# Kernel optimization log

Hardware: AMD Instinct MI355X
Metric: run time of the kernel (lower is better)

The kernel has to match this reference:

```python
import jax, jax.numpy as jnp
import numpy as np

BIG = 1e30  # stand-in for +inf at DP boundaries (never selected by min)


def setup_inputs() -> dict:
    key = jax.random.key(0)
    kx, kp = jax.random.split(key)
    B, D, T = 32, 16, 1024        # batch, channels (d_patts), stream length
    P, L = 64, 32                 # n_patts, l_patts
    x = jax.random.normal(kx, (B, D, T), dtype=jnp.float32)
    patts = jax.random.normal(kp, (P, D, L), dtype=jnp.float32)
    rho = 0.5
    w = float(rho ** (1.0 / L))   # self.w = rho ** (1 / l_patts)
    return {"x": x, "patts": patts, "w": w}


def _dtw(x, patts, w):
    # Weighted streaming DTW: for each pattern p and each ending time j,
    # D[i, j] = cost[i, j] + min(D[i-1, j], w*D[i, j-1], w*D[i-1, j-1])
    # with D[i, 0] = cost[i, 0] + D[i-1, 0] (first time column cumsum) and
    # cost[i, j] = ||x[:, j] - patts[:, i]||^2 (squared euclidean over channels).
    B, D, T = x.shape
    P, _, L = patts.shape
    p2 = jnp.sum(patts * patts, axis=1)                       # (P, L)

    def cost_at(xj):                                          # xj: (B, D)
        x2 = jnp.sum(xj * xj, axis=1)                         # (B,)
        xp = jnp.einsum('bd,pdl->bpl', xj, patts)             # (B, P, L)
        return x2[:, None, None] + p2[None] - 2.0 * xp        # (B, P, L)

    # first time column
    col0 = jnp.cumsum(cost_at(x[:, :, 0]), axis=-1)           # (B, P, L)

    def step(prev, xj):
        cost = cost_at(xj)                                    # (B, P, L)
        prev_up = jnp.concatenate(
            [jnp.full_like(prev[..., :1], BIG), prev[..., :-1]], axis=-1)
        m = w * jnp.minimum(prev, prev_up)                    # (B, P, L)

        def inner(new_im1, cm):                               # scan along pattern axis
            c_i, m_i = cm
            new_i = c_i + jnp.minimum(new_im1, m_i)
            return new_i, new_i

        _, new = jax.lax.scan(
            inner, jnp.full((B, P), BIG, cost.dtype),
            (jnp.moveaxis(cost, -1, 0), jnp.moveaxis(m, -1, 0)))
        new_col = jnp.moveaxis(new, 0, -1)                    # (B, P, L)
        return new_col, new_col[..., -1]                      # emit full-pattern match cost

    xs = jnp.moveaxis(x[:, :, 1:], -1, 0)                     # (T-1, B, D)
    _, rest = jax.lax.scan(step, col0, xs)                    # (T-1, B, P)
    dtw = jnp.concatenate([col0[None, ..., -1], rest], axis=0)  # (T, B, P)
    return jnp.moveaxis(dtw, 0, -1)                           # (B, P, T)


def reference(x, patts, w):
    return jnp.sqrt(_dtw(x, patts, w))
```

## Files before the change

kernel.cpp:

```cpp
#include <hip/hip_runtime.h>
#include <math.h>

#define B_ 32
#define D_ 16
#define T_ 1024
#define P_ 64
#define L_ 32
#define KB 524288.0f

typedef short short8 __attribute__((ext_vector_type(8)));
typedef float f32x4 __attribute__((ext_vector_type(4)));
typedef unsigned short ushort_t;

template<int CTRL, int ROW_MASK, bool BC>
__device__ __forceinline__ float dpp_mov(float old_, float src) {
  int o = __builtin_bit_cast(int, old_);
  int s = __builtin_bit_cast(int, src);
  int r = __builtin_amdgcn_update_dpp(o, s, CTRL, ROW_MASK, 0xf, BC);
  return __builtin_bit_cast(float, r);
}

__device__ __forceinline__ float scan_sum32(float v) {
  v += dpp_mov<0x111, 0xf, true>(0.f, v);
  v += dpp_mov<0x112, 0xf, true>(0.f, v);
  v += dpp_mov<0x114, 0xf, true>(0.f, v);
  v += dpp_mov<0x118, 0xf, true>(0.f, v);
  v += dpp_mov<0x142, 0xa, false>(0.f, v);
  return v;
}

__device__ __forceinline__ float scan_max32(float v) {
  asm("s_nop 1\n\t"
      "v_max_f32_dpp %0, %0, %0 row_shr:1 row_mask:0xf bank_mask:0xf\n\t"
      "s_nop 1\n\t"
      "v_max_f32_dpp %0, %0, %0 row_shr:2 row_mask:0xf bank_mask:0xf\n\t"
      "s_nop 1\n\t"
      "v_max_f32_dpp %0, %0, %0 row_shr:4 row_mask:0xf bank_mask:0xf\n\t"
      "s_nop 1\n\t"
      "v_max_f32_dpp %0, %0, %0 row_shr:8 row_mask:0xf bank_mask:0xf\n\t"
      "s_nop 1\n\t"
      "v_max_f32_dpp %0, %0, %0 row_bcast:15 row_mask:0xa bank_mask:0xf"
      : "+v"(v));
  return v;
}

__device__ __forceinline__ ushort_t f2bf(float f) {
  unsigned u = __builtin_bit_cast(unsigned, f);
  return (ushort_t)((u + 0x7FFFu + ((u >> 16) & 1u)) >> 16);
}
__device__ __forceinline__ float bf2f(ushort_t h) {
  unsigned u = ((unsigned)h) << 16;
  return __builtin_bit_cast(float, u);
}

__global__ __launch_bounds__(256) void prep_fused(
    const float* __restrict__ x, const float* __restrict__ patts,
    ushort_t* __restrict__ xA, ushort_t* __restrict__ pB) {
  const int bid = blockIdx.x;
  if (bid < 128) {
    int gid = bid * 256 + threadIdx.x;
    int b = gid >> 10, t = gid & 1023;
    float x2 = 0.f;
    ushort_t o[32];
#pragma unroll
    for (int d = 0; d < 16; ++d) {
      float v = x[((b * 16 + d) << 10) + t];
      x2 = fmaf(v, v, x2);
      o[d] = f2bf(v);
    }
    o[16] = 0x3F80; o[17] = 0x3F80;
    ushort_t hi = f2bf(x2);
    o[18] = hi;
    o[19] = f2bf(x2 - bf2f(hi));
#pragma unroll
    for (int d = 20; d < 32; ++d) o[d] = 0;
    uint4* dst = (uint4*)(xA + (size_t)gid * 32);
#pragma unroll
    for (int q = 0; q < 4; ++q) {
      const ushort_t* s = o + q * 8;
      uint4 u;
      u.x = (unsigned)s[0] | ((unsigned)s[1] << 16);
      u.y = (unsigned)s[2] | ((unsigned)s[3] << 16);
      u.z = (unsigned)s[4] | ((unsigned)s[5] << 16);
      u.w = (unsigned)s[6] | ((unsigned)s[7] << 16);
      dst[q] = u;
    }
  } else {
    __shared__ float Ls[4][16 * 33];
    __shared__ float Lh[4][64];
    __shared__ float LP2[4][32];
    const int sub = threadIdx.x >> 6;
    const int l = threadIdx.x & 63;
    const int p = (bid - 128) * 4 + sub;
    const int half = l >> 5;
    const int m = l & 31;

    float p2acc = 0.f;
#pragma unroll
    for (int dd = 0; dd < 16; dd += 2) {
      int d = dd + half;
      float v = patts[((p * 16 + d) << 5) + m];
      p2acc = fmaf(v, v, p2acc);
      Ls[sub][d * 33 + m] = scan_sum32(v);
    }
    Lh[sub][l] = p2acc;
    __syncthreads();
    {
      float tot = Lh[sub][m] + Lh[sub][32 + m];
      float pref = scan_sum32(tot);
      if (half == 0) LP2[sub][m] = pref;
    }
    __syncthreads();

    const int n = l & 15, q = l >> 4;
#pragma unroll
    for (int iblk = 0; iblk < 2; ++iblk) {
      const int i = iblk * 16 + n;
      ushort_t o[8];
      if (q < 2) {
#pragma unroll
        for (int e = 0; e < 8; ++e)
          o[e] = f2bf(-2.f * Ls[sub][(q * 8 + e) * 33 + i]);
      } else if (q == 2) {
        float P2 = LP2[sub][i];
        ushort_t hi = f2bf(P2);
        o[0] = hi; o[1] = f2bf(P2 - bf2f(hi));
        o[2] = f2bf((float)(i + 1)); o[3] = o[2];
        o[4] = o[5] = o[6] = o[7] = 0;
      } else {
#pragma unroll
        for (int e = 0; e < 8; ++e) o[e] = 0;
      }
      uint4 u;
      u.x = (unsigned)o[0] | ((unsigned)o[1] << 16);
      u.y = (unsigned)o[2] | ((unsigned)o[3] << 16);
      u.z = (unsigned)o[4] | ((unsigned)o[5] << 16);
      u.w = (unsigned)o[6] | ((unsigned)o[7] << 16);
      ((uint4*)pB)[(p * 2 + iblk) * 64 + l] = u;
    }
  }
}

__global__ __launch_bounds__(256, 4) void dtw_kernel(
    const ushort_t* __restrict__ xA,
    const ushort_t* __restrict__ pBg,
    const float* __restrict__ wp,
    float* __restrict__ out)
{
  __shared__ float lds[4 * 1320];

  const int tid = threadIdx.x;
  const int l   = tid & 63;
  const int wid = tid >> 6;
  const int li  = l & 31;
  const int g   = l >> 5;
  const int q4  = l >> 4;
  const unsigned bx = blockIdx.x;
  const int ch   = bx & 3u;
  const unsigned rest = bx >> 2;
  const int b     = rest >> 3;
  const int pbase = (rest & 7) << 3;
  const int pA  = pbase + (wid << 1);
  const float w = wp[0];
  const float nw = -w;
  const bool l0c = (li == 0), l31 = (li == 31);

  const int S0    = ch * 12;
  const int nT    = 28;
  const int warmT = ch ? 16 : 0;

  const short8* pBs = (const short8*)pBg;
  short8 B00 = pBs[((pA    ) * 2 + 0) * 64 + l];
  short8 B01 = pBs[((pA    ) * 2 + 1) * 64 + l];
  short8 B10 = pBs[((pA + 1) * 2 + 0) * 64 + l];
  short8 B11 = pBs[((pA + 1) * 2 + 1) * 64 + l];

  const short8* xAs = (const short8*)xA + ((size_t)b << 12);

  short8 Aa;
  auto loadA = [&](int t) {
    Aa = xAs[((((S0 + t) << 4) + (l & 15)) << 2) + q4];
  };

  float* base = lds + wid * 1320;
  float* ldsW = base + 20 + (l & 15) * 20 + q4 * 4;
  const float* ldsR  = base + 20 + g * 660 + li * 20;
  const float* ldsRx = ldsR - 20;

  if (l < 20) { base[l] = KB; base[660 + l] = KB; }
  __syncthreads();

  const f32x4 zk = {KB, KB, KB, KB};

  auto fill = [&]() {
    f32x4 d0 = __builtin_amdgcn_mfma_f32_16x16x32_bf16(Aa, B00, zk, 0, 0, 0);
    f32x4 d1 = __builtin_amdgcn_mfma_f32_16x16x32_bf16(Aa, B01, zk, 0, 0, 0);
    f32x4 d2 = __builtin_amdgcn_mfma_f32_16x16x32_bf16(Aa, B10, zk, 0, 0, 0);
    f32x4 d3 = __builtin_amdgcn_mfma_f32_16x16x32_bf16(Aa, B11, zk, 0, 0, 0);
    *(f32x4*)(ldsW + 0)   = d0;
    *(f32x4*)(ldsW + 320) = d1;
    *(f32x4*)(ldsW + 660) = d2;
    *(f32x4*)(ldsW + 980) = d3;
  };

  float* orow = out + (((size_t)(b * P_ + pA + g)) << 10) + (S0 << 4);
  float dcur = 0.f;

  loadA(0);
  fill();
  loadA(1);

  for (int t = 0; t < nT; ++t) {
    f32x4 s0 = *(const f32x4*)(ldsR + 0);
    f32x4 x0 = *(const f32x4*)(ldsRx + 0);
    f32x4 s1 = *(const f32x4*)(ldsR + 4);
    f32x4 x1 = *(const f32x4*)(ldsRx + 4);
    f32x4 s2 = *(const f32x4*)(ldsR + 8);
    f32x4 x2 = *(const f32x4*)(ldsRx + 8);
    f32x4 s3 = *(const f32x4*)(ldsR + 12);
    f32x4 x3 = *(const f32x4*)(ldsRx + 12);

    if (t + 1 < nT) fill();
    if (t + 2 < nT) loadA(t + 2);

    const bool first = (t == 0);
    const bool store = (t >= warmT);
    float* op = orow + (t << 4);

    float4 r0, r1, r2, r3;
#pragma unroll
    for (int k4 = 0; k4 < 4; ++k4) {
      f32x4 Sq = (k4 == 0) ? s0 : (k4 == 1) ? s1 : (k4 == 2) ? s2 : s3;
      f32x4 Xq = (k4 == 0) ? x0 : (k4 == 1) ? x1 : (k4 == 2) ? x2 : x3;
      float4 rv;
#pragma unroll
      for (int e = 0; e < 4; ++e) {
        float Zo = Sq[e];
        float Zx = Xq[e];
        float a = fmaf(nw, dcur, Zx);
        float c = fmaf(nw, dcur, Zo);
        float u;
        asm("s_nop 1\n\t"
            "v_max_f32_dpp %0, %1, %2 wave_shr:1 row_mask:0xf bank_mask:0xf"
            : "=&v"(u) : "v"(c), "v"(a));
        u = l0c ? a : u;
        float Mx = scan_max32(u);
        float val = Zo - Mx;
        if (first && k4 == 0 && e == 0)
          val = Zo - KB;
        dcur = val;
        if (e == 0) rv.x = val; else if (e == 1) rv.y = val;
        else if (e == 2) rv.z = val; else rv.w = val;
      }
      if (k4 == 0) r0 = rv; else if (k4 == 1) r1 = rv;
      else if (k4 == 2) r2 = rv; else r3 = rv;
    }
    if (store) {
      if (l31) {
        float4 s;
        s.x = __builtin_amdgcn_sqrtf(r0.x); s.y = __builtin_amdgcn_sqrtf(r0.y);
        s.z = __builtin_amdgcn_sqrtf(r0.z); s.w = __builtin_amdgcn_sqrtf(r0.w);
        *(float4*)(op + 0) = s;
        s.x = __builtin_amdgcn_sqrtf(r1.x); s.y = __builtin_amdgcn_sqrtf(r1.y);
        s.z = __builtin_amdgcn_sqrtf(r1.z); s.w = __builtin_amdgcn_sqrtf(r1.w);
        *(float4*)(op + 4) = s;
        s.x = __builtin_amdgcn_sqrtf(r2.x); s.y = __builtin_amdgcn_sqrtf(r2.y);
        s.z = __builtin_amdgcn_sqrtf(r2.z); s.w = __builtin_amdgcn_sqrtf(r2.w);
        *(float4*)(op + 8) = s;
        s.x = __builtin_amdgcn_sqrtf(r3.x); s.y = __builtin_amdgcn_sqrtf(r3.y);
        s.z = __builtin_amdgcn_sqrtf(r3.z); s.w = __builtin_amdgcn_sqrtf(r3.w);
        *(float4*)(op + 12) = s;
      }
    }
  }
}

extern "C" void kernel_launch(void* const* d_in, const int* in_sizes, int n_in,
                              void* d_out, int out_size, void* d_ws, size_t ws_size,
                              hipStream_t stream) {
  const float* x     = (const float*)d_in[0];
  const float* patts = (const float*)d_in[1];
  const float* w     = (const float*)d_in[2];
  float* out = (float*)d_out;

  ushort_t* xA = (ushort_t*)d_ws;
  ushort_t* pB = (ushort_t*)((char*)d_ws + (size_t)B_ * T_ * 32 * 2);

  prep_fused<<<144, 256, 0, stream>>>(x, patts, xA, pB);
  dtw_kernel<<<B_ * (P_ / 8) * 4, 256, 0, stream>>>(xA, pB, w, out);
}
```

Before: 109.8 us.

## Interleave two independent DTW chains per wave to hide DPP latency

Each wave now processes four patterns as two independent recurrence chains, interleaving their DPP max-scans so one chain's instructions fill the other's data-dependency hazard slots. The s_nop padding drops to zero between paired DPP ops. The grid halves, LDS per block doubles, and the launch-bounds occupancy hint drops from 4 to 2. The cost is fewer waves across the GPU (1024 blocks become 512) and higher register pressure.

```diff
diff --git a/kernel.cpp b/kernel.cpp
--- a/kernel.cpp
+++ b/kernel.cpp
@@ -29,19 +29,23 @@
   return v;
 }
 
-__device__ __forceinline__ float scan_max32(float v) {
+__device__ __forceinline__ void scan_max32_x2(float& u, float& v) {
   asm("s_nop 1\n\t"
       "v_max_f32_dpp %0, %0, %0 row_shr:1 row_mask:0xf bank_mask:0xf\n\t"
-      "s_nop 1\n\t"
+      "v_max_f32_dpp %1, %1, %1 row_shr:1 row_mask:0xf bank_mask:0xf\n\t"
+      "s_nop 0\n\t"
       "v_max_f32_dpp %0, %0, %0 row_shr:2 row_mask:0xf bank_mask:0xf\n\t"
-      "s_nop 1\n\t"
+      "v_max_f32_dpp %1, %1, %1 row_shr:2 row_mask:0xf bank_mask:0xf\n\t"
+      "s_nop 0\n\t"
       "v_max_f32_dpp %0, %0, %0 row_shr:4 row_mask:0xf bank_mask:0xf\n\t"
-      "s_nop 1\n\t"
+      "v_max_f32_dpp %1, %1, %1 row_shr:4 row_mask:0xf bank_mask:0xf\n\t"
+      "s_nop 0\n\t"
       "v_max_f32_dpp %0, %0, %0 row_shr:8 row_mask:0xf bank_mask:0xf\n\t"
-      "s_nop 1\n\t"
-      "v_max_f32_dpp %0, %0, %0 row_bcast:15 row_mask:0xa bank_mask:0xf"
-      : "+v"(v));
-  return v;
+      "v_max_f32_dpp %1, %1, %1 row_shr:8 row_mask:0xf bank_mask:0xf\n\t"
+      "s_nop 0\n\t"
+      "v_max_f32_dpp %0, %0, %0 row_bcast:15 row_mask:0xa bank_mask:0xf\n\t"
+      "v_max_f32_dpp %1, %1, %1 row_bcast:15 row_mask:0xa bank_mask:0xf"
+      : "+v"(u), "+v"(v));
 }
 
 __device__ __forceinline__ ushort_t f2bf(float f) {
@@ -141,13 +145,13 @@
   }
 }
 
-__global__ __launch_bounds__(256, 4) void dtw_kernel(
+__global__ __launch_bounds__(256, 2) void dtw_kernel(
     const ushort_t* __restrict__ xA,
     const ushort_t* __restrict__ pBg,
     const float* __restrict__ wp,
     float* __restrict__ out)
 {
-  __shared__ float lds[4 * 1320];
+  __shared__ float lds[4 * 2640];
 
   const int tid = threadIdx.x;
   const int l   = tid & 63;
@@ -158,9 +162,9 @@
   const unsigned bx = blockIdx.x;
   const int ch   = bx & 3u;
   const unsigned rest = bx >> 2;
-  const int b     = rest >> 3;
-  const int pbase = (rest & 7) << 3;
-  const int pA  = pbase + (wid << 1);
+  const int b     = rest >> 2;
+  const int pbase = (rest & 3) << 4;
+  const int pA0   = pbase + (wid << 2);
   const float w = wp[0];
   const float nw = -w;
   const bool l0c = (li == 0), l31 = (li == 31);
@@ -170,10 +174,14 @@
   const int warmT = ch ? 16 : 0;
 
   const short8* pBs = (const short8*)pBg;
-  short8 B00 = pBs[((pA    ) * 2 + 0) * 64 + l];
-  short8 B01 = pBs[((pA    ) * 2 + 1) * 64 + l];
-  short8 B10 = pBs[((pA + 1) * 2 + 0) * 64 + l];
-  short8 B11 = pBs[((pA + 1) * 2 + 1) * 64 + l];
+  short8 B00 = pBs[((pA0    ) * 2 + 0) * 64 + l];
+  short8 B01 = pBs[((pA0    ) * 2 + 1) * 64 + l];
+  short8 B10 = pBs[((pA0 + 1) * 2 + 0) * 64 + l];
+  short8 B11 = pBs[((pA0 + 1) * 2 + 1) * 64 + l];
+  short8 B20 = pBs[((pA0 + 2) * 2 + 0) * 64 + l];
+  short8 B21 = pBs[((pA0 + 2) * 2 + 1) * 64 + l];
+  short8 B30 = pBs[((pA0 + 3) * 2 + 0) * 64 + l];
+  short8 B31 = pBs[((pA0 + 3) * 2 + 1) * 64 + l];
 
   const short8* xAs = (const short8*)xA + ((size_t)b << 12);
 
@@ -182,12 +190,16 @@
     Aa = xAs[((((S0 + t) << 4) + (l & 15)) << 2) + q4];
   };
 
-  float* base = lds + wid * 1320;
+  float* base = lds + wid * 2640;
   float* ldsW = base + 20 + (l & 15) * 20 + q4 * 4;
-  const float* ldsR  = base + 20 + g * 660 + li * 20;
-  const float* ldsRx = ldsR - 20;
-
-  if (l < 20) { base[l] = KB; base[660 + l] = KB; }
+  const float* ldsRA  = base + 20 + g * 660 + li * 20;
+  const float* ldsRxA = ldsRA - 20;
+  const float* ldsRB  = ldsRA + 1320;
+  const float* ldsRxB = ldsRB - 20;
+
+  if (l < 20) {
+    base[l] = KB; base[660 + l] = KB; base[1320 + l] = KB; base[1980 + l] = KB;
+  }
   __syncthreads();
 
   const f32x4 zk = {KB, KB, KB, KB};
@@ -197,79 +209,123 @@
     f32x4 d1 = __builtin_amdgcn_mfma_f32_16x16x32_bf16(Aa, B01, zk, 0, 0, 0);
     f32x4 d2 = __builtin_amdgcn_mfma_f32_16x16x32_bf16(Aa, B10, zk, 0, 0, 0);
     f32x4 d3 = __builtin_amdgcn_mfma_f32_16x16x32_bf16(Aa, B11, zk, 0, 0, 0);
-    *(f32x4*)(ldsW + 0)   = d0;
-    *(f32x4*)(ldsW + 320) = d1;
-    *(f32x4*)(ldsW + 660) = d2;
-    *(f32x4*)(ldsW + 980) = d3;
+    f32x4 d4 = __builtin_amdgcn_mfma_f32_16x16x32_bf16(Aa, B20, zk, 0, 0, 0);
+    f32x4 d5 = __builtin_amdgcn_mfma_f32_16x16x32_bf16(Aa, B21, zk, 0, 0, 0);
+    f32x4 d6 = __builtin_amdgcn_mfma_f32_16x16x32_bf16(Aa, B30, zk, 0, 0, 0);
+    f32x4 d7 = __builtin_amdgcn_mfma_f32_16x16x32_bf16(Aa, B31, zk, 0, 0, 0);
+    *(f32x4*)(ldsW + 0)    = d0;
+    *(f32x4*)(ldsW + 320)  = d1;
+    *(f32x4*)(ldsW + 660)  = d2;
+    *(f32x4*)(ldsW + 980)  = d3;
+    *(f32x4*)(ldsW + 1320) = d4;
+    *(f32x4*)(ldsW + 1640) = d5;
+    *(f32x4*)(ldsW + 1980) = d6;
+    *(f32x4*)(ldsW + 2300) = d7;
   };
 
-  float* orow = out + (((size_t)(b * P_ + pA + g)) << 10) + (S0 << 4);
-  float dcur = 0.f;
+  float* orowA = out + (((size_t)(b * P_ + pA0 + g)) << 10) + (S0 << 4);
+  float* orowB = orowA + (2 << 10);
+  float dcurA = 0.f, dcurB = 0.f;
 
   loadA(0);
   fill();
   loadA(1);
 
   for (int t = 0; t < nT; ++t) {
-    f32x4 s0 = *(const f32x4*)(ldsR + 0);
-    f32x4 x0 = *(const f32x4*)(ldsRx + 0);
-    f32x4 s1 = *(const f32x4*)(ldsR + 4);
-    f32x4 x1 = *(const f32x4*)(ldsRx + 4);
-    f32x4 s2 = *(const f32x4*)(ldsR + 8);
-    f32x4 x2 = *(const f32x4*)(ldsRx + 8);
-    f32x4 s3 = *(const f32x4*)(ldsR + 12);
-    f32x4 x3 = *(const f32x4*)(ldsRx + 12);
+    f32x4 sA0 = *(const f32x4*)(ldsRA  + 0);
+    f32x4 xA0 = *(const f32x4*)(ldsRxA + 0);
+    f32x4 sB0 = *(const f32x4*)(ldsRB  + 0);
+    f32x4 xB0 = *(const f32x4*)(ldsRxB + 0);
+    f32x4 sA1 = *(const f32x4*)(ldsRA  + 4);
+    f32x4 xA1 = *(const f32x4*)(ldsRxA + 4);
+    f32x4 sB1 = *(const f32x4*)(ldsRB  + 4);
+    f32x4 xB1 = *(const f32x4*)(ldsRxB + 4);
+    f32x4 sA2 = *(const f32x4*)(ldsRA  + 8);
+    f32x4 xA2 = *(const f32x4*)(ldsRxA + 8);
+    f32x4 sB2 = *(const f32x4*)(ldsRB  + 8);
+    f32x4 xB2 = *(const f32x4*)(ldsRxB + 8);
+    f32x4 sA3 = *(const f32x4*)(ldsRA  + 12);
+    f32x4 xA3 = *(const f32x4*)(ldsRxA + 12);
+    f32x4 sB3 = *(const f32x4*)(ldsRB  + 12);
+    f32x4 xB3 = *(const f32x4*)(ldsRxB + 12);
 
     if (t + 1 < nT) fill();
     if (t + 2 < nT) loadA(t + 2);
 
     const bool first = (t == 0);
     const bool store = (t >= warmT);
-    float* op = orow + (t << 4);
-
-    float4 r0, r1, r2, r3;
+
+    float4 rA0, rA1, rA2, rA3, rB0, rB1, rB2, rB3;
 #pragma unroll
     for (int k4 = 0; k4 < 4; ++k4) {
-      f32x4 Sq = (k4 == 0) ? s0 : (k4 == 1) ? s1 : (k4 == 2) ? s2 : s3;
-      f32x4 Xq = (k4 == 0) ? x0 : (k4 == 1) ? x1 : (k4 == 2) ? x2 : x3;
-      float4 rv;
+      f32x4 SqA = (k4 == 0) ? sA0 : (k4 == 1) ? sA1 : (k4 == 2) ? sA2 : sA3;
+      f32x4 XqA = (k4 == 0) ? xA0 : (k4 == 1) ? xA1 : (k4 == 2) ? xA2 : xA3;
+      f32x4 SqB = (k4 == 0) ? sB0 : (k4 == 1) ? sB1 : (k4 == 2) ? sB2 : sB3;
+      f32x4 XqB = (k4 == 0) ? xB0 : (k4 == 1) ? xB1 : (k4 == 2) ? xB2 : xB3;
+      float4 rvA, rvB;
 #pragma unroll
       for (int e = 0; e < 4; ++e) {
-        float Zo = Sq[e];
-        float Zx = Xq[e];
-        float a = fmaf(nw, dcur, Zx);
-        float c = fmaf(nw, dcur, Zo);
-        float u;
+        float ZoA = SqA[e], ZxA = XqA[e];
+        float ZoB = SqB[e], ZxB = XqB[e];
+        float aA = fmaf(nw, dcurA, ZxA);
+        float cA = fmaf(nw, dcurA, ZoA);
+        float aB = fmaf(nw, dcurB, ZxB);
+        float cB = fmaf(nw, dcurB, ZoB);
+        float uA, uB;
         asm("s_nop 1\n\t"
-            "v_max_f32_dpp %0, %1, %2 wave_shr:1 row_mask:0xf bank_mask:0xf"
-            : "=&v"(u) : "v"(c), "v"(a));
-        u = l0c ? a : u;
-        float Mx = scan_max32(u);
-        float val = Zo - Mx;
-        if (first && k4 == 0 && e == 0)
-          val = Zo - KB;
-        dcur = val;
-        if (e == 0) rv.x = val; else if (e == 1) rv.y = val;
-        else if (e == 2) rv.z = val; else rv.w = val;
+            "v_max_f32_dpp %0, %2, %3 wave_shr:1 row_mask:0xf bank_mask:0xf\n\t"
+            "v_max_f32_dpp %1, %4, %5 wave_shr:1 row_mask:0xf bank_mask:0xf"
+            : "=&v"(uA), "=&v"(uB)
+            : "v"(cA), "v"(aA), "v"(cB), "v"(aB));
+        uA = l0c ? aA : uA;
+        uB = l0c ? aB : uB;
+        scan_max32_x2(uA, uB);
+        float vA = ZoA - uA;
+        float vB = ZoB - uB;
+        if (first && k4 == 0 && e == 0) {
+          vA = ZoA - KB;
+          vB = ZoB - KB;
+        }
+        dcurA = vA; dcurB = vB;
+        if (e == 0) { rvA.x = vA; rvB.x = vB; }
+        else if (e == 1) { rvA.y = vA; rvB.y = vB; }
+        else if (e == 2) { rvA.z = vA; rvB.z = vB; }
+        else { rvA.w = vA; rvB.w = vB; }
       }
-      if (k4 == 0) r0 = rv; else if (k4 == 1) r1 = rv;
-      else if (k4 == 2) r2 = rv; else r3 = rv;
+      if (k4 == 0) { rA0 = rvA; rB0 = rvB; }
+      else if (k4 == 1) { rA1 = rvA; rB1 = rvB; }
+      else if (k4 == 2) { rA2 = rvA; rB2 = rvB; }
+      else { rA3 = rvA; rB3 = rvB; }
     }
     if (store) {
       if (l31) {
+        float* opA = orowA + (t << 4);
+        float* opB = orowB + (t << 4);
         float4 s;
-        s.x = __builtin_amdgcn_sqrtf(r0.x); s.y = __builtin_amdgcn_sqrtf(r0.y);
-        s.z = __builtin_amdgcn_sqrtf(r0.z); s.w = __builtin_amdgcn_sqrtf(r0.w);
-        *(float4*)(op + 0) = s;
-        s.x = __builtin_amdgcn_sqrtf(r1.x); s.y = __builtin_amdgcn_sqrtf(r1.y);
-        s.z = __builtin_amdgcn_sqrtf(r1.z); s.w = __builtin_amdgcn_sqrtf(r1.w);
-        *(float4*)(op + 4) = s;
-        s.x = __builtin_amdgcn_sqrtf(r2.x); s.y = __builtin_amdgcn_sqrtf(r2.y);
-        s.z = __builtin_amdgcn_sqrtf(r2.z); s.w = __builtin_amdgcn_sqrtf(r2.w);
-        *(float4*)(op + 8) = s;
-        s.x = __builtin_amdgcn_sqrtf(r3.x); s.y = __builtin_amdgcn_sqrtf(r3.y);
-        s.z = __builtin_amdgcn_sqrtf(r3.z); s.w = __builtin_amdgcn_sqrtf(r3.w);
-        *(float4*)(op + 12) = s;
+        s.x = __builtin_amdgcn_sqrtf(rA0.x); s.y = __builtin_amdgcn_sqrtf(rA0.y);
+        s.z = __builtin_amdgcn_sqrtf(rA0.z); s.w = __builtin_amdgcn_sqrtf(rA0.w);
+        *(float4*)(opA + 0) = s;
+        s.x = __builtin_amdgcn_sqrtf(rA1.x); s.y = __builtin_amdgcn_sqrtf(rA1.y);
+        s.z = __builtin_amdgcn_sqrtf(rA1.z); s.w = __builtin_amdgcn_sqrtf(rA1.w);
+        *(float4*)(opA + 4) = s;
+        s.x = __builtin_amdgcn_sqrtf(rA2.x); s.y = __builtin_amdgcn_sqrtf(rA2.y);
+        s.z = __builtin_amdgcn_sqrtf(rA2.z); s.w = __builtin_amdgcn_sqrtf(rA2.w);
+        *(float4*)(opA + 8) = s;
+        s.x = __builtin_amdgcn_sqrtf(rA3.x); s.y = __builtin_amdgcn_sqrtf(rA3.y);
+        s.z = __builtin_amdgcn_sqrtf(rA3.z); s.w = __builtin_amdgcn_sqrtf(rA3.w);
+        *(float4*)(opA + 12) = s;
+        s.x = __builtin_amdgcn_sqrtf(rB0.x); s.y = __builtin_amdgcn_sqrtf(rB0.y);
+        s.z = __builtin_amdgcn_sqrtf(rB0.z); s.w = __builtin_amdgcn_sqrtf(rB0.w);
+        *(float4*)(opB + 0) = s;
+        s.x = __builtin_amdgcn_sqrtf(rB1.x); s.y = __builtin_amdgcn_sqrtf(rB1.y);
+        s.z = __builtin_amdgcn_sqrtf(rB1.z); s.w = __builtin_amdgcn_sqrtf(rB1.w);
+        *(float4*)(opB + 4) = s;
+        s.x = __builtin_amdgcn_sqrtf(rB2.x); s.y = __builtin_amdgcn_sqrtf(rB2.y);
+        s.z = __builtin_amdgcn_sqrtf(rB2.z); s.w = __builtin_amdgcn_sqrtf(rB2.w);
+        *(float4*)(opB + 8) = s;
+        s.x = __builtin_amdgcn_sqrtf(rB3.x); s.y = __builtin_amdgcn_sqrtf(rB3.y);
+        s.z = __builtin_amdgcn_sqrtf(rB3.z); s.w = __builtin_amdgcn_sqrtf(rB3.w);
+        *(float4*)(opB + 12) = s;
       }
     }
   }
@@ -287,5 +343,5 @@
   ushort_t* pB = (ushort_t*)((char*)d_ws + (size_t)B_ * T_ * 32 * 2);
 
   prep_fused<<<144, 256, 0, stream>>>(x, patts, xA, pB);
-  dtw_kernel<<<B_ * (P_ / 8) * 4, 256, 0, stream>>>(xA, pB, w, out);
-}
+  dtw_kernel<<<B_ * (P_ / 16) * 4, 256, 0, stream>>>(xA, pB, w, out);
+}
```

Result: slower. 114.3 us (+4.1%).

## Fuse bf16 prep into DTW kernel, building MFMA operands in registers

Applied to the files above, without the earlier changes.

Removes the separate prep kernel and its workspace round trip. Each wave now builds its pattern B operands (prefix-summed, scaled, packed to bf16) at kernel start, and builds the x A operand on the fly from fp32 x with a deeper software-pipelined load. This drops one kernel launch and the global write and read of the packed data. In exchange, every block redundantly recomputes the pattern preprocessing, and the per-step A build adds ALU work and strided global loads to the serial loop.

```diff
diff --git a/kernel.cpp b/kernel.cpp
--- a/kernel.cpp
+++ b/kernel.cpp
@@ -53,97 +53,9 @@
   return __builtin_bit_cast(float, u);
 }
 
-__global__ __launch_bounds__(256) void prep_fused(
-    const float* __restrict__ x, const float* __restrict__ patts,
-    ushort_t* __restrict__ xA, ushort_t* __restrict__ pB) {
-  const int bid = blockIdx.x;
-  if (bid < 128) {
-    int gid = bid * 256 + threadIdx.x;
-    int b = gid >> 10, t = gid & 1023;
-    float x2 = 0.f;
-    ushort_t o[32];
-#pragma unroll
-    for (int d = 0; d < 16; ++d) {
-      float v = x[((b * 16 + d) << 10) + t];
-      x2 = fmaf(v, v, x2);
-      o[d] = f2bf(v);
-    }
-    o[16] = 0x3F80; o[17] = 0x3F80;
-    ushort_t hi = f2bf(x2);
-    o[18] = hi;
-    o[19] = f2bf(x2 - bf2f(hi));
-#pragma unroll
-    for (int d = 20; d < 32; ++d) o[d] = 0;
-    uint4* dst = (uint4*)(xA + (size_t)gid * 32);
-#pragma unroll
-    for (int q = 0; q < 4; ++q) {
-      const ushort_t* s = o + q * 8;
-      uint4 u;
-      u.x = (unsigned)s[0] | ((unsigned)s[1] << 16);
-      u.y = (unsigned)s[2] | ((unsigned)s[3] << 16);
-      u.z = (unsigned)s[4] | ((unsigned)s[5] << 16);
-      u.w = (unsigned)s[6] | ((unsigned)s[7] << 16);
-      dst[q] = u;
-    }
-  } else {
-    __shared__ float Ls[4][16 * 33];
-    __shared__ float Lh[4][64];
-    __shared__ float LP2[4][32];
-    const int sub = threadIdx.x >> 6;
-    const int l = threadIdx.x & 63;
-    const int p = (bid - 128) * 4 + sub;
-    const int half = l >> 5;
-    const int m = l & 31;
-
-    float p2acc = 0.f;
-#pragma unroll
-    for (int dd = 0; dd < 16; dd += 2) {
-      int d = dd + half;
-      float v = patts[((p * 16 + d) << 5) + m];
-      p2acc = fmaf(v, v, p2acc);
-      Ls[sub][d * 33 + m] = scan_sum32(v);
-    }
-    Lh[sub][l] = p2acc;
-    __syncthreads();
-    {
-      float tot = Lh[sub][m] + Lh[sub][32 + m];
-      float pref = scan_sum32(tot);
-      if (half == 0) LP2[sub][m] = pref;
-    }
-    __syncthreads();
-
-    const int n = l & 15, q = l >> 4;
-#pragma unroll
-    for (int iblk = 0; iblk < 2; ++iblk) {
-      const int i = iblk * 16 + n;
-      ushort_t o[8];
-      if (q < 2) {
-#pragma unroll
-        for (int e = 0; e < 8; ++e)
-          o[e] = f2bf(-2.f * Ls[sub][(q * 8 + e) * 33 + i]);
-      } else if (q == 2) {
-        float P2 = LP2[sub][i];
-        ushort_t hi = f2bf(P2);
-        o[0] = hi; o[1] = f2bf(P2 - bf2f(hi));
-        o[2] = f2bf((float)(i + 1)); o[3] = o[2];
-        o[4] = o[5] = o[6] = o[7] = 0;
-      } else {
-#pragma unroll
-        for (int e = 0; e < 8; ++e) o[e] = 0;
-      }
-      uint4 u;
-      u.x = (unsigned)o[0] | ((unsigned)o[1] << 16);
-      u.y = (unsigned)o[2] | ((unsigned)o[3] << 16);
-      u.z = (unsigned)o[4] | ((unsigned)o[5] << 16);
-      u.w = (unsigned)o[6] | ((unsigned)o[7] << 16);
-      ((uint4*)pB)[(p * 2 + iblk) * 64 + l] = u;
-    }
-  }
-}
-
-__global__ __launch_bounds__(256, 4) void dtw_kernel(
-    const ushort_t* __restrict__ xA,
-    const ushort_t* __restrict__ pBg,
+__global__ __launch_bounds__(256, 4) void dtw_fused(
+    const float* __restrict__ x,
+    const float* __restrict__ patts,
     const float* __restrict__ wp,
     float* __restrict__ out)
 {
@@ -169,34 +81,102 @@
   const int nT    = 28;
   const int warmT = ch ? 16 : 0;
 
-  const short8* pBs = (const short8*)pBg;
-  short8 B00 = pBs[((pA    ) * 2 + 0) * 64 + l];
-  short8 B01 = pBs[((pA    ) * 2 + 1) * 64 + l];
-  short8 B10 = pBs[((pA + 1) * 2 + 0) * 64 + l];
-  short8 B11 = pBs[((pA + 1) * 2 + 1) * 64 + l];
-
-  const short8* xAs = (const short8*)xA + ((size_t)b << 12);
-
+  float* base = lds + wid * 1320;
+
+  short8 Bf[2][2];
+  {
+    const int m = li;
+    const int n = l & 15;
+#pragma unroll
+    for (int p2 = 0; p2 < 2; ++p2) {
+      const int p = pA + p2;
+      float p2acc = 0.f;
+#pragma unroll
+      for (int dd = 0; dd < 16; dd += 2) {
+        int d = dd + g;
+        float v = patts[(((p << 4) + d) << 5) + m];
+        p2acc = fmaf(v, v, p2acc);
+        base[d * 33 + m] = scan_sum32(v);
+      }
+      float tot  = p2acc + __shfl_xor(p2acc, 32, 64);
+      float pref = scan_sum32(tot);
+#pragma unroll
+      for (int iblk = 0; iblk < 2; ++iblk) {
+        const int i = iblk * 16 + n;
+        float P2 = __shfl(pref, i, 64);
+        ushort_t o[8];
+        if (q4 < 2) {
+#pragma unroll
+          for (int e = 0; e < 8; ++e)
+            o[e] = f2bf(-2.f * base[(q4 * 8 + e) * 33 + i]);
+        } else if (q4 == 2) {
+          ushort_t hi = f2bf(P2);
+          o[0] = hi; o[1] = f2bf(P2 - bf2f(hi));
+          o[2] = f2bf((float)(i + 1)); o[3] = o[2];
+          o[4] = o[5] = o[6] = o[7] = 0;
+        } else {
+#pragma unroll
+          for (int e = 0; e < 8; ++e) o[e] = 0;
+        }
+        int4 u;
+        u.x = (int)((unsigned)o[0] | ((unsigned)o[1] << 16));
+        u.y = (int)((unsigned)o[2] | ((unsigned)o[3] << 16));
+        u.z = (int)((unsigned)o[4] | ((unsigned)o[5] << 16));
+        u.w = (int)((unsigned)o[6] | ((unsigned)o[7] << 16));
+        Bf[p2][iblk] = __builtin_bit_cast(short8, u);
+      }
+    }
+  }
+
+  if (l < 20) { base[l] = KB; base[660 + l] = KB; }
+  __syncthreads();
+
+  const float* xb = x + ((size_t)b << 14);
+  float xr[8] = {0.f, 0.f, 0.f, 0.f, 0.f, 0.f, 0.f, 0.f};
+  auto loadX = [&](int t) {
+    if (l < 32) {
+      const int j = ((S0 + t) << 4) + (l & 15);
+      const float* col = xb + (q4 << 13) + j;
+#pragma unroll
+      for (int e = 0; e < 8; ++e) xr[e] = col[e << 10];
+    }
+  };
   short8 Aa;
-  auto loadA = [&](int t) {
-    Aa = xAs[((((S0 + t) << 4) + (l & 15)) << 2) + q4];
+  auto buildA = [&]() {
+    float part = 0.f;
+#pragma unroll
+    for (int e = 0; e < 8; ++e) part = fmaf(xr[e], xr[e], part);
+    float pa = __shfl(part, (l & 15), 64);
+    float pb = __shfl(part, (l & 15) + 16, 64);
+    float x2 = pa + pb;
+    unsigned u0, u1, u2, u3;
+    if (q4 < 2) {
+      u0 = (unsigned)f2bf(xr[0]) | ((unsigned)f2bf(xr[1]) << 16);
+      u1 = (unsigned)f2bf(xr[2]) | ((unsigned)f2bf(xr[3]) << 16);
+      u2 = (unsigned)f2bf(xr[4]) | ((unsigned)f2bf(xr[5]) << 16);
+      u3 = (unsigned)f2bf(xr[6]) | ((unsigned)f2bf(xr[7]) << 16);
+    } else if (q4 == 2) {
+      ushort_t hi = f2bf(x2);
+      ushort_t lo = f2bf(x2 - bf2f(hi));
+      u0 = 0x3F803F80u;
+      u1 = (unsigned)hi | ((unsigned)lo << 16);
+      u2 = 0u; u3 = 0u;
+    } else { u0 = u1 = u2 = u3 = 0u; }
+    int4 ui; ui.x = (int)u0; ui.y = (int)u1; ui.z = (int)u2; ui.w = (int)u3;
+    Aa = __builtin_bit_cast(short8, ui);
   };
 
-  float* base = lds + wid * 1320;
   float* ldsW = base + 20 + (l & 15) * 20 + q4 * 4;
   const float* ldsR  = base + 20 + g * 660 + li * 20;
   const float* ldsRx = ldsR - 20;
 
-  if (l < 20) { base[l] = KB; base[660 + l] = KB; }
-  __syncthreads();
-
   const f32x4 zk = {KB, KB, KB, KB};
 
   auto fill = [&]() {
-    f32x4 d0 = __builtin_amdgcn_mfma_f32_16x16x32_bf16(Aa, B00, zk, 0, 0, 0);
-    f32x4 d1 = __builtin_amdgcn_mfma_f32_16x16x32_bf16(Aa, B01, zk, 0, 0, 0);
-    f32x4 d2 = __builtin_amdgcn_mfma_f32_16x16x32_bf16(Aa, B10, zk, 0, 0, 0);
-    f32x4 d3 = __builtin_amdgcn_mfma_f32_16x16x32_bf16(Aa, B11, zk, 0, 0, 0);
+    f32x4 d0 = __builtin_amdgcn_mfma_f32_16x16x32_bf16(Aa, Bf[0][0], zk, 0, 0, 0);
+    f32x4 d1 = __builtin_amdgcn_mfma_f32_16x16x32_bf16(Aa, Bf[0][1], zk, 0, 0, 0);
+    f32x4 d2 = __builtin_amdgcn_mfma_f32_16x16x32_bf16(Aa, Bf[1][0], zk, 0, 0, 0);
+    f32x4 d3 = __builtin_amdgcn_mfma_f32_16x16x32_bf16(Aa, Bf[1][1], zk, 0, 0, 0);
     *(f32x4*)(ldsW + 0)   = d0;
     *(f32x4*)(ldsW + 320) = d1;
     *(f32x4*)(ldsW + 660) = d2;
@@ -206,9 +186,10 @@
   float* orow = out + (((size_t)(b * P_ + pA + g)) << 10) + (S0 << 4);
   float dcur = 0.f;
 
-  loadA(0);
+  loadX(0); buildA();
   fill();
-  loadA(1);
+  loadX(1); buildA();
+  loadX(2);
 
   for (int t = 0; t < nT; ++t) {
     f32x4 s0 = *(const f32x4*)(ldsR + 0);
@@ -216,12 +197,13 @@
     f32x4 s1 = *(const f32x4*)(ldsR + 4);
     f32x4 x1 = *(const f32x4*)(ldsRx + 4);
     f32x4 s2 = *(const f32x4*)(ldsR + 8);
-    f32x4 x2 = *(const f32x4*)(ldsRx + 8);
+    f32x4 x2q = *(const f32x4*)(ldsRx + 8);
     f32x4 s3 = *(const f32x4*)(ldsR + 12);
     f32x4 x3 = *(const f32x4*)(ldsRx + 12);
 
     if (t + 1 < nT) fill();
-    if (t + 2 < nT) loadA(t + 2);
+    if (t + 2 < nT) buildA();
+    if (t + 3 < nT) loadX(t + 3);
 
     const bool first = (t == 0);
     const bool store = (t >= warmT);
@@ -231,7 +213,7 @@
 #pragma unroll
     for (int k4 = 0; k4 < 4; ++k4) {
       f32x4 Sq = (k4 == 0) ? s0 : (k4 == 1) ? s1 : (k4 == 2) ? s2 : s3;
-      f32x4 Xq = (k4 == 0) ? x0 : (k4 == 1) ? x1 : (k4 == 2) ? x2 : x3;
+      f32x4 Xq = (k4 == 0) ? x0 : (k4 == 1) ? x1 : (k4 == 2) ? x2q : x3;
       float4 rv;
 #pragma unroll
       for (int e = 0; e < 4; ++e) {
@@ -283,9 +265,5 @@
   const float* w     = (const float*)d_in[2];
   float* out = (float*)d_out;
 
-  ushort_t* xA = (ushort_t*)d_ws;
-  ushort_t* pB = (ushort_t*)((char*)d_ws + (size_t)B_ * T_ * 32 * 2);
-
-  prep_fused<<<144, 256, 0, stream>>>(x, patts, xA, pB);
-  dtw_kernel<<<B_ * (P_ / 8) * 4, 256, 0, stream>>>(xA, pB, w, out);
-}
+  dtw_fused<<<B_ * 8 * 4, 256, 0, stream>>>(x, patts, w, out);
+}
```

New measurement: 119.7 us. 1.09x slower.
